# Kernel tuning notes

Measured on AMD Instinct MI355X. Metric: run time of the kernel, lower is better.

Reference implementation:

```python
import jax, jax.numpy as jnp
import numpy as np

ARAP_WEIGHT = 1.0


def _decoder(code, W1, b1, W2, b2, W3, b3):
    # code: [D] -> vertices [N, 3]
    h = jax.nn.relu(code @ W1 + b1)
    h = jax.nn.relu(h @ W2 + b2)
    v = h @ W3 + b3
    return v.reshape(-1, 3)


def _arap_per_vertex(xyz1, recon, nbr, num_nbr, wmat):
    # xyz1, recon: [N,3]; nbr: [N,K] int; num_nbr: [N]; wmat: [N,K]
    N, K = nbr.shape
    mask = (jnp.arange(K)[None, :] < num_nbr[:, None]).astype(wmat.dtype)
    w = wmat * mask                              # zero out padded neighbors
    e_rest = xyz1[nbr] - xyz1[:, None, :]        # [N,K,3] rest-pose edges (gather)
    e_def = recon[nbr] - recon[:, None, :]       # [N,K,3] deformed edges (gather)
    # weighted covariance per vertex: S_i = sum_k w_ik e_ik e'_ik^T  -> [N,3,3]
    S = jnp.einsum('nk,nka,nkb->nab', w, e_rest, e_def)
    U, _, Vt = jnp.linalg.svd(S)
    V = jnp.swapaxes(Vt, -1, -2)
    R0 = jnp.einsum('nab,ncb->nac', V, U)        # V U^T
    d = jnp.linalg.det(R0)                       # reflection fix
    diag = jnp.stack([jnp.ones_like(d), jnp.ones_like(d), d], axis=-1)  # [N,3]
    R = jnp.einsum('nab,nb,ncb->nac', V, diag, U)
    R = jax.lax.stop_gradient(R)                 # local-global: rotations fixed in bwd
    e_rot = jnp.einsum('nab,nkb->nka', R, e_rest)
    resid = e_def - e_rot
    return jnp.sum(w * jnp.sum(resid * resid, axis=-1), axis=-1)  # [N]


def setup_inputs() -> dict:
    key = jax.random.key(0)
    ks = jax.random.split(key, 12)
    N, K, D = 20000, 16, 256
    H1, H2 = 512, 1024
    inp = {
        'code': jax.random.normal(ks[0], (D,), jnp.float32),
        'xyz1': jax.random.normal(ks[1], (N, 3), jnp.float32),
        'weightMatrix': jax.random.uniform(ks[2], (N, K), jnp.float32),
        'W1': jax.random.normal(ks[3], (D, H1), jnp.float32) * (1.0 / np.sqrt(D)),
        'b1': jax.random.normal(ks[4], (H1,), jnp.float32) * 0.01,
        'W2': jax.random.normal(ks[5], (H1, H2), jnp.float32) * (1.0 / np.sqrt(H1)),
        'b2': jax.random.normal(ks[6], (H2,), jnp.float32) * 0.01,
        'W3': jax.random.normal(ks[7], (H2, N * 3), jnp.float32) * (1.0 / np.sqrt(H2)),
        'b3': jax.random.normal(ks[8], (N * 3,), jnp.float32) * 0.01,
        'neighborsMatrix': jax.random.randint(ks[9], (N, K), 0, N, jnp.int64),
        'numNeighbors': jax.random.randint(ks[10], (N,), 0, 17, jnp.int64),
    }
    return inp


def reference(code, xyz1, weightMatrix, W1, b1, W2, b2, W3, b3,
              neighborsMatrix, numNeighbors):
    def energy(c):
        recon = _decoder(c, W1, b1, W2, b2, W3, b3)
        pv = _arap_per_vertex(xyz1, recon, neighborsMatrix, numNeighbors, weightMatrix)
        return ARAP_WEIGHT * jnp.mean(pv)

    E, g = jax.value_and_grad(energy)(code)
    # torch module returns (arapEnergy.item(), -code.grad) with arapEnergy = -E
    return (-E, g)
```

## Files before the change

### kernel.cpp

```cpp
#include <hip/hip_runtime.h>
#include <hip/hip_bf16.h>

#define N_V   20000
#define KNB   16
#define DCODE 256
#define H1    512
#define H2    1024
#define M3    60000

#define OFF_L2P   0
#define OFF_VPART 8192
#define OFF_V     488192
#define OFF_GV    548192
#define OFF_GZ2   608192
#define OFF_GZ1   609216
#define OFF_H1    609728
#define OFF_H2    610240
#define OFF_HC    611264
#define OFF_LIST  612288
#define OFF_CNT   613312
#define OFF_E     613316

__global__ void k_mlp12(const float* __restrict__ code, const float* __restrict__ W1,
                        const float* __restrict__ b1, const float* __restrict__ W2,
                        float* __restrict__ ws) {
    __shared__ float red[4][64];
    __shared__ float h1s[64];
    int t = threadIdx.x;
    int bx = blockIdx.x, dz = blockIdx.y;
    int d0 = dz * 64;

    int ln = t & 63, g = t >> 6;
    {
        float acc = 0.f;
        int r0 = g * 64;
#pragma unroll 8
        for (int rr = 0; rr < 64; ++rr)
            acc += code[r0 + rr] * W1[(size_t)(r0 + rr) * H1 + d0 + ln];
        red[g][ln] = acc;
    }
    __syncthreads();
    if (g == 0) {
        float h = fmaxf(red[0][ln] + red[1][ln] + red[2][ln] + red[3][ln] + b1[d0 + ln], 0.f);
        h1s[ln] = h;
        if (bx == 0) ws[OFF_H1 + d0 + ln] = h;
    }
    __syncthreads();

    int m = bx * 256 + t;
    float acc = 0.f;
#pragma unroll 8
    for (int dd = 0; dd < 64; ++dd)
        acc += h1s[dd] * W2[(size_t)(d0 + dd) * H2 + m];
    ws[OFF_L2P + dz * H2 + m] = acc;

    int gid = (dz * 4 + bx) * 256 + t;
    for (int idx = gid; idx < M3; idx += 8192) ws[OFF_GV + idx] = 0.f;
    if (gid == 0) { ws[OFF_E] = 0.f; ws[OFF_E + 1] = 0.f; }
}

__global__ void k_compact(const float* __restrict__ b2, float* __restrict__ ws) {
    __shared__ int scan[256];
    int t = threadIdx.x;
    float h[4]; int c = 0;
#pragma unroll
    for (int q = 0; q < 4; ++q) {
        int j = t * 4 + q;
        float s = b2[j];
#pragma unroll
        for (int p = 0; p < 8; ++p) s += ws[OFF_L2P + p * H2 + j];
        float hv = fmaxf(s, 0.f);
        ws[OFF_H2 + j] = hv;
        ws[OFF_GZ2 + j] = 0.f;
        h[q] = hv;
        c += (hv > 0.f) ? 1 : 0;
    }
    scan[t] = c;
    __syncthreads();
    for (int off = 1; off < 256; off <<= 1) {
        int x = (t >= off) ? scan[t - off] : 0;
        __syncthreads();
        scan[t] += x;
        __syncthreads();
    }
    int base = scan[t] - c;
    int* list = reinterpret_cast<int*>(&ws[OFF_LIST]);
#pragma unroll
    for (int q = 0; q < 4; ++q) {
        if (h[q] > 0.f) {
            list[base] = t * 4 + q;
            ws[OFF_HC + base] = h[q];
            ++base;
        }
    }
    if (t == 255) *reinterpret_cast<int*>(&ws[OFF_CNT]) = scan[255];
}

__global__ void k_l3p(const float* __restrict__ W3, float* __restrict__ ws) {
    __shared__ int   rlist[128];
    __shared__ float rh[128];
    int jz = blockIdx.y;
    int cnt = *reinterpret_cast<const int*>(&ws[OFF_CNT]);
    int per = (cnt + 7) >> 3;
    int s0 = jz * per;
    int s1 = s0 + per; if (s1 > cnt) s1 = cnt;
    int n = s1 - s0;
    int t = threadIdx.x;
    if (t < 128 && t < n) {
        rlist[t] = reinterpret_cast<const int*>(&ws[OFF_LIST])[s0 + t];
        rh[t]    = ws[OFF_HC + s0 + t];
    }
    __syncthreads();
    int m4 = blockIdx.x * 1024 + t * 4;
    if (m4 >= M3) return;
    float ax = 0.f, ay = 0.f, az = 0.f, aw = 0.f;
    int ii = 0;
    for (; ii + 7 < n; ii += 8) {
        float4 wv[8];
#pragma unroll
        for (int u = 0; u < 8; ++u)
            wv[u] = *reinterpret_cast<const float4*>(&W3[(size_t)rlist[ii + u] * M3 + m4]);
#pragma unroll
        for (int u = 0; u < 8; ++u) {
            float h = rh[ii + u];
            ax += h * wv[u].x; ay += h * wv[u].y; az += h * wv[u].z; aw += h * wv[u].w;
        }
    }
    for (; ii < n; ++ii) {
        float h = rh[ii];
        float4 wv = *reinterpret_cast<const float4*>(&W3[(size_t)rlist[ii] * M3 + m4]);
        ax += h * wv.x; ay += h * wv.y; az += h * wv.z; aw += h * wv.w;
    }
    *reinterpret_cast<float4*>(&ws[OFF_VPART + jz * M3 + m4]) =
        make_float4(ax, ay, az, aw);
}

__global__ void k_vred(const float* __restrict__ b3, float* __restrict__ ws) {
    int i4 = blockIdx.x * 256 + threadIdx.x;
    if (i4 < M3 / 4) {
        int m = i4 * 4;
        float4 a = *reinterpret_cast<const float4*>(&b3[m]);
#pragma unroll
        for (int jz = 0; jz < 8; ++jz) {
            float4 p = *reinterpret_cast<const float4*>(&ws[OFF_VPART + jz * M3 + m]);
            a.x += p.x; a.y += p.y; a.z += p.z; a.w += p.w;
        }
        *reinterpret_cast<float4*>(&ws[OFF_V + m]) = a;
    }
}


__device__ inline void jrotf(float a[3][3], float v[3][3], int p, int q) {
    float apq = a[p][q];
    if (fabsf(apq) < 1e-30f) return;
    float theta = (a[q][q] - a[p][p]) / (2.0f * apq);
    float t;
    if (fabsf(theta) > 1e18f) t = 0.5f / theta;
    else t = copysignf(1.0f, theta) / (fabsf(theta) + sqrtf(theta * theta + 1.0f));
    float c = 1.0f / sqrtf(t * t + 1.0f);
    float s = t * c;
    float app = a[p][p], aqq = a[q][q];
    a[p][p] = app - t * apq;
    a[q][q] = aqq + t * apq;
    a[p][q] = 0.0f; a[q][p] = 0.0f;
    int r = 3 - p - q;
    float arp = a[r][p], arq = a[r][q];
    a[r][p] = c * arp - s * arq; a[p][r] = a[r][p];
    a[r][q] = s * arp + c * arq; a[q][r] = a[r][q];
#pragma unroll
    for (int k2 = 0; k2 < 3; ++k2) {
        float vkp = v[k2][p], vkq = v[k2][q];
        v[k2][p] = c * vkp - s * vkq;
        v[k2][q] = s * vkp + c * vkq;
    }
}

__device__ void compute_Rf(const float S[3][3], float R[3][3]) {
    float A[3][3], V[3][3];
#pragma unroll
    for (int a = 0; a < 3; ++a)
#pragma unroll
        for (int b = 0; b < 3; ++b) {
            float s = 0.0f;
#pragma unroll
            for (int c = 0; c < 3; ++c) s += S[c][a] * S[c][b];
            A[a][b] = s;
            V[a][b] = (a == b) ? 1.0f : 0.0f;
        }
    for (int sweep = 0; sweep < 15; ++sweep) {
        float off = A[0][1]*A[0][1] + A[0][2]*A[0][2] + A[1][2]*A[1][2];
        float dg  = A[0][0]*A[0][0] + A[1][1]*A[1][1] + A[2][2]*A[2][2];
        if (off <= 1e-12f * (dg + 1e-30f)) break;
        jrotf(A, V, 0, 1); jrotf(A, V, 0, 2); jrotf(A, V, 1, 2);
    }
    int id[3] = {0, 1, 2};
    if (A[id[0]][id[0]] < A[id[1]][id[1]]) { int t = id[0]; id[0] = id[1]; id[1] = t; }
    if (A[id[0]][id[0]] < A[id[2]][id[2]]) { int t = id[0]; id[0] = id[2]; id[2] = t; }
    if (A[id[1]][id[1]] < A[id[2]][id[2]]) { int t = id[1]; id[1] = id[2]; id[2] = t; }
    float v0[3], v1[3], v2[3];
#pragma unroll
    for (int r = 0; r < 3; ++r) {
        v0[r] = V[r][id[0]]; v1[r] = V[r][id[1]]; v2[r] = V[r][id[2]];
    }
    float u0[3], u1[3], u2[3];
#pragma unroll
    for (int a = 0; a < 3; ++a)
        u0[a] = S[a][0]*v0[0] + S[a][1]*v0[1] + S[a][2]*v0[2];
    float n0 = sqrtf(u0[0]*u0[0] + u0[1]*u0[1] + u0[2]*u0[2]);
    if (!(n0 > 1e-20f)) {
#pragma unroll
        for (int a = 0; a < 3; ++a)
#pragma unroll
            for (int c = 0; c < 3; ++c) R[a][c] = (a == c) ? 1.0f : 0.0f;
        return;
    }
#pragma unroll
    for (int a = 0; a < 3; ++a) u0[a] /= n0;
    float t1[3];
#pragma unroll
    for (int a = 0; a < 3; ++a)
        t1[a] = S[a][0]*v1[0] + S[a][1]*v1[1] + S[a][2]*v1[2];
    float dp = u0[0]*t1[0] + u0[1]*t1[1] + u0[2]*t1[2];
#pragma unroll
    for (int a = 0; a < 3; ++a) t1[a] -= dp * u0[a];
    float n1 = sqrtf(t1[0]*t1[0] + t1[1]*t1[1] + t1[2]*t1[2]);
    if (n1 > 1e-5f * n0) {
#pragma unroll
        for (int a = 0; a < 3; ++a) u1[a] = t1[a] / n1;
    } else {
        int m = (fabsf(u0[0]) <= fabsf(u0[1]) && fabsf(u0[0]) <= fabsf(u0[2])) ? 0
              : (fabsf(u0[1]) <= fabsf(u0[2]) ? 1 : 2);
        float e[3] = {0.0f, 0.0f, 0.0f}; e[m] = 1.0f;
        float cx[3] = { u0[1]*e[2] - u0[2]*e[1],
                        u0[2]*e[0] - u0[0]*e[2],
                        u0[0]*e[1] - u0[1]*e[0] };
        float nn = sqrtf(cx[0]*cx[0] + cx[1]*cx[1] + cx[2]*cx[2]);
#pragma unroll
        for (int a = 0; a < 3; ++a) u1[a] = cx[a] / nn;
    }
    u2[0] = u0[1]*u1[2] - u0[2]*u1[1];
    u2[1] = u0[2]*u1[0] - u0[0]*u1[2];
    u2[2] = u0[0]*u1[1] - u0[1]*u1[0];
    float d = v0[0]*(v1[1]*v2[2] - v1[2]*v2[1])
            - v0[1]*(v1[0]*v2[2] - v1[2]*v2[0])
            + v0[2]*(v1[0]*v2[1] - v1[1]*v2[0]);
#pragma unroll
    for (int a = 0; a < 3; ++a)
#pragma unroll
        for (int c = 0; c < 3; ++c)
            R[a][c] = v0[a]*u0[c] + v1[a]*u1[c] + d * (v2[a]*u2[c]);
}

__global__ void k_arap(const float* __restrict__ xyz1, const float* __restrict__ wmat,
                       const int* __restrict__ nbr, const int* __restrict__ nnum,
                       float* __restrict__ ws) {
    const float* recon = ws + OFF_V;
    float* gv = ws + OFF_GV;
    int i = blockIdx.x * 256 + threadIdx.x;
    double pv = 0.0;
    if (i < N_V) {
        int num = nnum[i]; if (num > KNB) num = KNB;
        float cr0 = xyz1[3*i], cr1 = xyz1[3*i+1], cr2 = xyz1[3*i+2];
        float cd0 = recon[3*i], cd1 = recon[3*i+1], cd2 = recon[3*i+2];
        float er[KNB][3], ed[KNB][3], wk[KNB];
        int   jn[KNB];
        float S[3][3] = {{0,0,0},{0,0,0},{0,0,0}};
#pragma unroll
        for (int k = 0; k < KNB; ++k) {
            bool live = (k < num);
            int j = live ? nbr[i*KNB + k] : i;
            float w = live ? wmat[i*KNB + k] : 0.f;
            jn[k] = j; wk[k] = w;
            float e0 = xyz1[3*j]   - cr0, e1 = xyz1[3*j+1] - cr1, e2 = xyz1[3*j+2] - cr2;
            float f0 = recon[3*j]  - cd0, f1 = recon[3*j+1] - cd1, f2 = recon[3*j+2] - cd2;
            er[k][0] = e0; er[k][1] = e1; er[k][2] = e2;
            ed[k][0] = f0; ed[k][1] = f1; ed[k][2] = f2;
            S[0][0] += w*e0*f0; S[0][1] += w*e0*f1; S[0][2] += w*e0*f2;
            S[1][0] += w*e1*f0; S[1][1] += w*e1*f1; S[1][2] += w*e1*f2;
            S[2][0] += w*e2*f0; S[2][1] += w*e2*f1; S[2][2] += w*e2*f2;
        }
        float R[3][3];
        compute_Rf(S, R);
        const float gscale = 2.0f / (float)N_V;
        float own0 = 0.f, own1 = 0.f, own2 = 0.f;
#pragma unroll
        for (int k = 0; k < KNB; ++k) {
            if (k < num) {
                float w = wk[k];
                float r0 = ed[k][0] - (R[0][0]*er[k][0] + R[0][1]*er[k][1] + R[0][2]*er[k][2]);
                float r1 = ed[k][1] - (R[1][0]*er[k][0] + R[1][1]*er[k][1] + R[1][2]*er[k][2]);
                float r2 = ed[k][2] - (R[2][0]*er[k][0] + R[2][1]*er[k][1] + R[2][2]*er[k][2]);
                pv += (double)(w * (r0*r0 + r1*r1 + r2*r2));
                float g0 = gscale * w * r0;
                float g1 = gscale * w * r1;
                float g2 = gscale * w * r2;
                int j = jn[k];
                atomicAdd(&gv[3*j+0], g0);
                atomicAdd(&gv[3*j+1], g1);
                atomicAdd(&gv[3*j+2], g2);
                own0 += g0; own1 += g1; own2 += g2;
            }
        }
        if (num > 0) {
            atomicAdd(&gv[3*i+0], -own0);
            atomicAdd(&gv[3*i+1], -own1);
            atomicAdd(&gv[3*i+2], -own2);
        }
    }
#pragma unroll
    for (int m = 32; m; m >>= 1) pv += __shfl_xor(pv, m);
    __shared__ double wred[4];
    if ((threadIdx.x & 63) == 0) wred[threadIdx.x >> 6] = pv;
    __syncthreads();
    if (threadIdx.x == 0)
        atomicAdd(reinterpret_cast<double*>(ws + OFF_E),
                  wred[0] + wred[1] + wred[2] + wred[3]);
}


__global__ void k_gh2(const float* __restrict__ W3, float* __restrict__ ws) {
    int b = blockIdx.x;
    int cnt = *reinterpret_cast<const int*>(&ws[OFF_CNT]);
    if (2 * b >= cnt) return;
    const int* list = reinterpret_cast<const int*>(&ws[OFF_LIST]);
    int j0 = list[2 * b];
    bool has1 = (2 * b + 1 < cnt);
    int j1 = has1 ? list[2 * b + 1] : j0;
    const float4* w3r0 = reinterpret_cast<const float4*>(W3 + (size_t)j0 * M3);
    const float4* w3r1 = reinterpret_cast<const float4*>(W3 + (size_t)j1 * M3);
    const float4* gv4  = reinterpret_cast<const float4*>(ws + OFF_GV);
    float acc0 = 0.f, acc1 = 0.f;
    for (int it = threadIdx.x; it < M3 / 4; it += 256) {
        float4 g = gv4[it];
        float4 a = w3r0[it];
        float4 c = w3r1[it];
        acc0 += a.x*g.x + a.y*g.y + a.z*g.z + a.w*g.w;
        acc1 += c.x*g.x + c.y*g.y + c.z*g.z + c.w*g.w;
    }
    for (int m = 32; m; m >>= 1) {
        acc0 += __shfl_xor(acc0, m);
        acc1 += __shfl_xor(acc1, m);
    }
    __shared__ float wsum[4][2];
    if ((threadIdx.x & 63) == 0) {
        wsum[threadIdx.x >> 6][0] = acc0;
        wsum[threadIdx.x >> 6][1] = acc1;
    }
    __syncthreads();
    if (threadIdx.x == 0) {
        ws[OFF_GZ2 + j0] = wsum[0][0] + wsum[1][0] + wsum[2][0] + wsum[3][0];
        if (has1)
            ws[OFF_GZ2 + j1] = wsum[0][1] + wsum[1][1] + wsum[2][1] + wsum[3][1];
    }
}

__global__ void k_gh1(const float* __restrict__ W2, float* __restrict__ ws) {
    int wv = threadIdx.x >> 6, ln = threadIdx.x & 63;
    int i = blockIdx.x * 4 + wv;
    const float* gz2 = ws + OFF_GZ2;
    float acc = 0.f;
#pragma unroll
    for (int it = 0; it < H2 / 64; ++it) {
        int jj = ln + it * 64;
        acc += W2[(size_t)i * H2 + jj] * gz2[jj];
    }
    for (int m = 32; m; m >>= 1) acc += __shfl_xor(acc, m);
    if (ln == 0) ws[OFF_GZ1 + i] = (ws[OFF_H1 + i] > 0.f) ? acc : 0.f;
}

__global__ void k_gcode(const float* __restrict__ W1, float* __restrict__ ws,
                        float* __restrict__ out) {
    int wv = threadIdx.x >> 6, ln = threadIdx.x & 63;
    int d = blockIdx.x * 4 + wv;
    const float* gz1 = ws + OFF_GZ1;
    float acc = 0.f;
#pragma unroll
    for (int it = 0; it < H1 / 64; ++it) {
        int ii = ln + it * 64;
        acc += W1[(size_t)d * H1 + ii] * gz1[ii];
    }
    for (int m = 32; m; m >>= 1) acc += __shfl_xor(acc, m);
    if (ln == 0) out[1 + d] = acc;
    if (blockIdx.x == 0 && threadIdx.x == 0) {
        double E = *reinterpret_cast<const double*>(ws + OFF_E);
        out[0] = (float)(-(E / (double)N_V));
    }
}

extern "C" void kernel_launch(void* const* d_in, const int* in_sizes, int n_in,
                              void* d_out, int out_size, void* d_ws, size_t ws_size,
                              hipStream_t stream) {
    const float* code = (const float*)d_in[0];
    const float* xyz1 = (const float*)d_in[1];
    const float* wmat = (const float*)d_in[2];
    const float* W1   = (const float*)d_in[3];
    const float* b1   = (const float*)d_in[4];
    const float* W2   = (const float*)d_in[5];
    const float* b2   = (const float*)d_in[6];
    const float* W3   = (const float*)d_in[7];
    const float* b3   = (const float*)d_in[8];
    const int*   nbr  = (const int*)d_in[9];
    const int*   nnum = (const int*)d_in[10];
    float* out = (float*)d_out;
    float* ws  = (float*)d_ws;

    k_mlp12  <<<dim3(4, 8),  256, 0, stream>>>(code, W1, b1, W2, ws);
    k_compact<<<1,           256, 0, stream>>>(b2, ws);
    k_l3p    <<<dim3(59, 8), 256, 0, stream>>>(W3, ws);
    k_vred   <<<59,          256, 0, stream>>>(b3, ws);
    k_arap   <<<79,          256, 0, stream>>>(xyz1, wmat, nbr, nnum, ws);
    k_gh2    <<<512,         256, 0, stream>>>(W3, ws);
    k_gh1    <<<128,         256, 0, stream>>>(W2, ws);
    k_gcode  <<<64,          256, 0, stream>>>(W1, ws, out);
}
```

Before: 120.8 us.

## Fuse compaction into layer-3 GEMV, atomics for vertex sum, faster SVD, split gh2

Folds the single-block ReLU compaction into each k_l3p block, which now computes its own 128-row slice of h2. Partial vertex sums are accumulated into b3-initialised memory with atomics, which removes k_vred and the 8x60000 partial buffer. Also replaces the Jacobi convergence check with six fixed sweeps using hardware rcp/rsq, launches ARAP with 64-thread blocks for more blocks, and splits the gh2 reduction across two halves with unrolled accumulators. This trades two kernel launches and extra traffic for float atomic contention, non-deterministic summation order and slightly less accurate rotations.

```diff
diff --git a/kernel.cpp b/kernel.cpp
--- a/kernel.cpp
+++ b/kernel.cpp
@@ -9,21 +9,20 @@
 #define M3    60000
 
 #define OFF_L2P   0
-#define OFF_VPART 8192
-#define OFF_V     488192
-#define OFF_GV    548192
-#define OFF_GZ2   608192
-#define OFF_GZ1   609216
-#define OFF_H1    609728
-#define OFF_H2    610240
-#define OFF_HC    611264
-#define OFF_LIST  612288
-#define OFF_CNT   613312
-#define OFF_E     613316
+#define OFF_V     8192
+#define OFF_GV    68192
+#define OFF_GZ2P  128192
+#define OFF_GZ1   130240
+#define OFF_H1    130752
+#define OFF_H2    131264
+#define OFF_HC    132288
+#define OFF_LIST  133312
+#define OFF_CNT8  134336
+#define OFF_E     134344
 
 __global__ void k_mlp12(const float* __restrict__ code, const float* __restrict__ W1,
                         const float* __restrict__ b1, const float* __restrict__ W2,
-                        float* __restrict__ ws) {
+                        const float* __restrict__ b3, float* __restrict__ ws) {
     __shared__ float red[4][64];
     __shared__ float h1s[64];
     int t = threadIdx.x;
@@ -55,62 +54,56 @@
     ws[OFF_L2P + dz * H2 + m] = acc;
 
     int gid = (dz * 4 + bx) * 256 + t;
-    for (int idx = gid; idx < M3; idx += 8192) ws[OFF_GV + idx] = 0.f;
-    if (gid == 0) { ws[OFF_E] = 0.f; ws[OFF_E + 1] = 0.f; }
-}
-
-__global__ void k_compact(const float* __restrict__ b2, float* __restrict__ ws) {
-    __shared__ int scan[256];
+    for (int idx = gid; idx < M3; idx += 8192) {
+        ws[OFF_V + idx]  = b3[idx];
+        ws[OFF_GV + idx] = 0.f;
+    }
+    if (gid == 0) *reinterpret_cast<double*>(ws + OFF_E) = 0.0;
+}
+
+__global__ void k_l3p(const float* __restrict__ b2, const float* __restrict__ W3,
+                      float* __restrict__ ws) {
+    __shared__ float rh[128];
+    __shared__ int   rlist[128];
+    __shared__ int   scan[128];
     int t = threadIdx.x;
-    float h[4]; int c = 0;
-#pragma unroll
-    for (int q = 0; q < 4; ++q) {
-        int j = t * 4 + q;
-        float s = b2[j];
-#pragma unroll
-        for (int p = 0; p < 8; ++p) s += ws[OFF_L2P + p * H2 + j];
-        float hv = fmaxf(s, 0.f);
-        ws[OFF_H2 + j] = hv;
-        ws[OFF_GZ2 + j] = 0.f;
-        h[q] = hv;
-        c += (hv > 0.f) ? 1 : 0;
-    }
-    scan[t] = c;
+    int jz = blockIdx.y;
+    int rbase = jz * 128;
+
+    float hv = 0.f; int flag = 0;
+    if (t < 128) {
+        float s = b2[rbase + t];
+#pragma unroll
+        for (int p = 0; p < 8; ++p) s += ws[OFF_L2P + p * H2 + rbase + t];
+        hv = fmaxf(s, 0.f);
+        flag = (hv > 0.f) ? 1 : 0;
+        scan[t] = flag;
+    }
     __syncthreads();
-    for (int off = 1; off < 256; off <<= 1) {
-        int x = (t >= off) ? scan[t - off] : 0;
+    for (int off = 1; off < 128; off <<= 1) {
+        int x = 0;
+        if (t < 128 && t >= off) x = scan[t - off];
         __syncthreads();
-        scan[t] += x;
+        if (t < 128) scan[t] += x;
         __syncthreads();
     }
-    int base = scan[t] - c;
-    int* list = reinterpret_cast<int*>(&ws[OFF_LIST]);
-#pragma unroll
-    for (int q = 0; q < 4; ++q) {
-        if (h[q] > 0.f) {
-            list[base] = t * 4 + q;
-            ws[OFF_HC + base] = h[q];
-            ++base;
-        }
-    }
-    if (t == 255) *reinterpret_cast<int*>(&ws[OFF_CNT]) = scan[255];
-}
-
-__global__ void k_l3p(const float* __restrict__ W3, float* __restrict__ ws) {
-    __shared__ int   rlist[128];
-    __shared__ float rh[128];
-    int jz = blockIdx.y;
-    int cnt = *reinterpret_cast<const int*>(&ws[OFF_CNT]);
-    int per = (cnt + 7) >> 3;
-    int s0 = jz * per;
-    int s1 = s0 + per; if (s1 > cnt) s1 = cnt;
-    int n = s1 - s0;
-    int t = threadIdx.x;
-    if (t < 128 && t < n) {
-        rlist[t] = reinterpret_cast<const int*>(&ws[OFF_LIST])[s0 + t];
-        rh[t]    = ws[OFF_HC + s0 + t];
+    if (t < 128 && flag) {
+        int idx = scan[t] - 1;
+        rlist[idx] = rbase + t;
+        rh[idx] = hv;
+    }
+    if (blockIdx.x == 0 && t < 128) {
+        ws[OFF_H2 + rbase + t] = hv;
+        if (flag) {
+            reinterpret_cast<int*>(&ws[OFF_LIST])[jz * 128 + scan[t] - 1] = rbase + t;
+            ws[OFF_HC + jz * 128 + scan[t] - 1] = hv;
+        }
+        if (t == 127)
+            reinterpret_cast<int*>(&ws[OFF_CNT8])[jz] = scan[127];
     }
     __syncthreads();
+    int n = scan[127];
+
     int m4 = blockIdx.x * 1024 + t * 4;
     if (m4 >= M3) return;
     float ax = 0.f, ay = 0.f, az = 0.f, aw = 0.f;
@@ -131,33 +124,25 @@
         float4 wv = *reinterpret_cast<const float4*>(&W3[(size_t)rlist[ii] * M3 + m4]);
         ax += h * wv.x; ay += h * wv.y; az += h * wv.z; aw += h * wv.w;
     }
-    *reinterpret_cast<float4*>(&ws[OFF_VPART + jz * M3 + m4]) =
-        make_float4(ax, ay, az, aw);
-}
-
-__global__ void k_vred(const float* __restrict__ b3, float* __restrict__ ws) {
-    int i4 = blockIdx.x * 256 + threadIdx.x;
-    if (i4 < M3 / 4) {
-        int m = i4 * 4;
-        float4 a = *reinterpret_cast<const float4*>(&b3[m]);
-#pragma unroll
-        for (int jz = 0; jz < 8; ++jz) {
-            float4 p = *reinterpret_cast<const float4*>(&ws[OFF_VPART + jz * M3 + m]);
-            a.x += p.x; a.y += p.y; a.z += p.z; a.w += p.w;
-        }
-        *reinterpret_cast<float4*>(&ws[OFF_V + m]) = a;
-    }
-}
-
+    if (n > 0) {
+        atomicAdd(&ws[OFF_V + m4 + 0], ax);
+        atomicAdd(&ws[OFF_V + m4 + 1], ay);
+        atomicAdd(&ws[OFF_V + m4 + 2], az);
+        atomicAdd(&ws[OFF_V + m4 + 3], aw);
+    }
+}
+
+
+__device__ inline float frcp(float x) { return __builtin_amdgcn_rcpf(x); }
+__device__ inline float frsq(float x) { return __builtin_amdgcn_rsqf(x); }
 
 __device__ inline void jrotf(float a[3][3], float v[3][3], int p, int q) {
     float apq = a[p][q];
-    if (fabsf(apq) < 1e-30f) return;
-    float theta = (a[q][q] - a[p][p]) / (2.0f * apq);
-    float t;
-    if (fabsf(theta) > 1e18f) t = 0.5f / theta;
-    else t = copysignf(1.0f, theta) / (fabsf(theta) + sqrtf(theta * theta + 1.0f));
-    float c = 1.0f / sqrtf(t * t + 1.0f);
+    float den = 2.0f * apq;
+    float sden = copysignf(fmaxf(fabsf(den), 1e-30f), den);
+    float theta = (a[q][q] - a[p][p]) * frcp(sden);
+    float t = copysignf(1.0f, theta) * frcp(fabsf(theta) + sqrtf(theta * theta + 1.0f));
+    float c = frsq(t * t + 1.0f);
     float s = t * c;
     float app = a[p][p], aqq = a[q][q];
     a[p][p] = app - t * apq;
@@ -187,10 +172,7 @@
             A[a][b] = s;
             V[a][b] = (a == b) ? 1.0f : 0.0f;
         }
-    for (int sweep = 0; sweep < 15; ++sweep) {
-        float off = A[0][1]*A[0][1] + A[0][2]*A[0][2] + A[1][2]*A[1][2];
-        float dg  = A[0][0]*A[0][0] + A[1][1]*A[1][1] + A[2][2]*A[2][2];
-        if (off <= 1e-12f * (dg + 1e-30f)) break;
+    for (int sweep = 0; sweep < 6; ++sweep) {
         jrotf(A, V, 0, 1); jrotf(A, V, 0, 2); jrotf(A, V, 1, 2);
     }
     int id[3] = {0, 1, 2};
@@ -214,8 +196,9 @@
             for (int c = 0; c < 3; ++c) R[a][c] = (a == c) ? 1.0f : 0.0f;
         return;
     }
-#pragma unroll
-    for (int a = 0; a < 3; ++a) u0[a] /= n0;
+    float rn0 = frcp(n0);
+#pragma unroll
+    for (int a = 0; a < 3; ++a) u0[a] *= rn0;
     float t1[3];
 #pragma unroll
     for (int a = 0; a < 3; ++a)
@@ -225,8 +208,9 @@
     for (int a = 0; a < 3; ++a) t1[a] -= dp * u0[a];
     float n1 = sqrtf(t1[0]*t1[0] + t1[1]*t1[1] + t1[2]*t1[2]);
     if (n1 > 1e-5f * n0) {
-#pragma unroll
-        for (int a = 0; a < 3; ++a) u1[a] = t1[a] / n1;
+        float rn1 = frcp(n1);
+#pragma unroll
+        for (int a = 0; a < 3; ++a) u1[a] = t1[a] * rn1;
     } else {
         int m = (fabsf(u0[0]) <= fabsf(u0[1]) && fabsf(u0[0]) <= fabsf(u0[2])) ? 0
               : (fabsf(u0[1]) <= fabsf(u0[2]) ? 1 : 2);
@@ -234,9 +218,9 @@
         float cx[3] = { u0[1]*e[2] - u0[2]*e[1],
                         u0[2]*e[0] - u0[0]*e[2],
                         u0[0]*e[1] - u0[1]*e[0] };
-        float nn = sqrtf(cx[0]*cx[0] + cx[1]*cx[1] + cx[2]*cx[2]);
-#pragma unroll
-        for (int a = 0; a < 3; ++a) u1[a] = cx[a] / nn;
+        float rnn = frsq(cx[0]*cx[0] + cx[1]*cx[1] + cx[2]*cx[2]);
+#pragma unroll
+        for (int a = 0; a < 3; ++a) u1[a] = cx[a] * rnn;
     }
     u2[0] = u0[1]*u1[2] - u0[2]*u1[1];
     u2[1] = u0[2]*u1[0] - u0[0]*u1[2];
@@ -256,7 +240,7 @@
                        float* __restrict__ ws) {
     const float* recon = ws + OFF_V;
     float* gv = ws + OFF_GV;
-    int i = blockIdx.x * 256 + threadIdx.x;
+    int i = blockIdx.x * 64 + threadIdx.x;
     double pv = 0.0;
     if (i < N_V) {
         int num = nnum[i]; if (num > KNB) num = KNB;
@@ -271,8 +255,8 @@
             int j = live ? nbr[i*KNB + k] : i;
             float w = live ? wmat[i*KNB + k] : 0.f;
             jn[k] = j; wk[k] = w;
-            float e0 = xyz1[3*j]   - cr0, e1 = xyz1[3*j+1] - cr1, e2 = xyz1[3*j+2] - cr2;
-            float f0 = recon[3*j]  - cd0, f1 = recon[3*j+1] - cd1, f2 = recon[3*j+2] - cd2;
+            float e0 = xyz1[3*j]  - cr0, e1 = xyz1[3*j+1] - cr1, e2 = xyz1[3*j+2] - cr2;
+            float f0 = recon[3*j] - cd0, f1 = recon[3*j+1] - cd1, f2 = recon[3*j+2] - cd2;
             er[k][0] = e0; er[k][1] = e1; er[k][2] = e2;
             ed[k][0] = f0; ed[k][1] = f1; ed[k][2] = f2;
             S[0][0] += w*e0*f0; S[0][1] += w*e0*f1; S[0][2] += w*e0*f2;
@@ -309,60 +293,97 @@
     }
 #pragma unroll
     for (int m = 32; m; m >>= 1) pv += __shfl_xor(pv, m);
-    __shared__ double wred[4];
-    if ((threadIdx.x & 63) == 0) wred[threadIdx.x >> 6] = pv;
-    __syncthreads();
     if (threadIdx.x == 0)
-        atomicAdd(reinterpret_cast<double*>(ws + OFF_E),
-                  wred[0] + wred[1] + wred[2] + wred[3]);
+        atomicAdd(reinterpret_cast<double*>(ws + OFF_E), pv);
 }
 
 
 __global__ void k_gh2(const float* __restrict__ W3, float* __restrict__ ws) {
-    int b = blockIdx.x;
-    int cnt = *reinterpret_cast<const int*>(&ws[OFF_CNT]);
-    if (2 * b >= cnt) return;
+    const int* cnt8 = reinterpret_cast<const int*>(&ws[OFF_CNT8]);
+    int pre[9];
+    pre[0] = 0;
+#pragma unroll
+    for (int c = 0; c < 8; ++c) pre[c + 1] = pre[c] + cnt8[c];
+    int total = pre[8];
+    int g0 = 2 * blockIdx.x;
+    if (g0 >= total) return;
+    int g1 = g0 + 1;
+    bool has1 = (g1 < total);
+
     const int* list = reinterpret_cast<const int*>(&ws[OFF_LIST]);
-    int j0 = list[2 * b];
-    bool has1 = (2 * b + 1 < cnt);
-    int j1 = has1 ? list[2 * b + 1] : j0;
+    int c0 = 0, c1 = 0;
+#pragma unroll
+    for (int c = 0; c < 8; ++c) {
+        if (g0 >= pre[c + 1]) c0 = c + 1;
+        if (g1 >= pre[c + 1]) c1 = c + 1;
+    }
+    int j0 = list[c0 * 128 + (g0 - pre[c0])];
+    int j1 = has1 ? list[c1 * 128 + (g1 - pre[c1])] : j0;
+
+    int half = blockIdx.y;
+    int start = half * 7500;
+    int end = start + 7500;
     const float4* w3r0 = reinterpret_cast<const float4*>(W3 + (size_t)j0 * M3);
     const float4* w3r1 = reinterpret_cast<const float4*>(W3 + (size_t)j1 * M3);
     const float4* gv4  = reinterpret_cast<const float4*>(ws + OFF_GV);
-    float acc0 = 0.f, acc1 = 0.f;
-    for (int it = threadIdx.x; it < M3 / 4; it += 256) {
+    int t = threadIdx.x;
+
+    float a00 = 0.f, a01 = 0.f, a02 = 0.f, a03 = 0.f;
+    float a10 = 0.f, a11 = 0.f, a12 = 0.f, a13 = 0.f;
+    int it = start + t;
+    for (; it + 768 < end; it += 1024) {
+        float4 g0v = gv4[it],        g1v = gv4[it + 256],
+               g2v = gv4[it + 512],  g3v = gv4[it + 768];
+        float4 p0 = w3r0[it],        p1 = w3r0[it + 256],
+               p2 = w3r0[it + 512],  p3 = w3r0[it + 768];
+        float4 q0 = w3r1[it],        q1 = w3r1[it + 256],
+               q2 = w3r1[it + 512],  q3 = w3r1[it + 768];
+        a00 += p0.x*g0v.x + p0.y*g0v.y + p0.z*g0v.z + p0.w*g0v.w;
+        a01 += p1.x*g1v.x + p1.y*g1v.y + p1.z*g1v.z + p1.w*g1v.w;
+        a02 += p2.x*g2v.x + p2.y*g2v.y + p2.z*g2v.z + p2.w*g2v.w;
+        a03 += p3.x*g3v.x + p3.y*g3v.y + p3.z*g3v.z + p3.w*g3v.w;
+        a10 += q0.x*g0v.x + q0.y*g0v.y + q0.z*g0v.z + q0.w*g0v.w;
+        a11 += q1.x*g1v.x + q1.y*g1v.y + q1.z*g1v.z + q1.w*g1v.w;
+        a12 += q2.x*g2v.x + q2.y*g2v.y + q2.z*g2v.z + q2.w*g2v.w;
+        a13 += q3.x*g3v.x + q3.y*g3v.y + q3.z*g3v.z + q3.w*g3v.w;
+    }
+    for (; it < end; it += 256) {
         float4 g = gv4[it];
-        float4 a = w3r0[it];
-        float4 c = w3r1[it];
-        acc0 += a.x*g.x + a.y*g.y + a.z*g.z + a.w*g.w;
-        acc1 += c.x*g.x + c.y*g.y + c.z*g.z + c.w*g.w;
-    }
+        float4 p = w3r0[it];
+        float4 q = w3r1[it];
+        a00 += p.x*g.x + p.y*g.y + p.z*g.z + p.w*g.w;
+        a10 += q.x*g.x + q.y*g.y + q.z*g.z + q.w*g.w;
+    }
+    float acc0 = a00 + a01 + a02 + a03;
+    float acc1 = a10 + a11 + a12 + a13;
     for (int m = 32; m; m >>= 1) {
         acc0 += __shfl_xor(acc0, m);
         acc1 += __shfl_xor(acc1, m);
     }
     __shared__ float wsum[4][2];
-    if ((threadIdx.x & 63) == 0) {
-        wsum[threadIdx.x >> 6][0] = acc0;
-        wsum[threadIdx.x >> 6][1] = acc1;
+    if ((t & 63) == 0) {
+        wsum[t >> 6][0] = acc0;
+        wsum[t >> 6][1] = acc1;
     }
     __syncthreads();
-    if (threadIdx.x == 0) {
-        ws[OFF_GZ2 + j0] = wsum[0][0] + wsum[1][0] + wsum[2][0] + wsum[3][0];
+    if (t == 0) {
+        float* gz2p = ws + OFF_GZ2P + half * H2;
+        gz2p[j0] = wsum[0][0] + wsum[1][0] + wsum[2][0] + wsum[3][0];
         if (has1)
-            ws[OFF_GZ2 + j1] = wsum[0][1] + wsum[1][1] + wsum[2][1] + wsum[3][1];
+            gz2p[j1] = wsum[0][1] + wsum[1][1] + wsum[2][1] + wsum[3][1];
     }
 }
 
 __global__ void k_gh1(const float* __restrict__ W2, float* __restrict__ ws) {
     int wv = threadIdx.x >> 6, ln = threadIdx.x & 63;
     int i = blockIdx.x * 4 + wv;
-    const float* gz2 = ws + OFF_GZ2;
     float acc = 0.f;
 #pragma unroll
     for (int it = 0; it < H2 / 64; ++it) {
         int jj = ln + it * 64;
-        acc += W2[(size_t)i * H2 + jj] * gz2[jj];
+        float gz2 = (ws[OFF_H2 + jj] > 0.f)
+                  ? (ws[OFF_GZ2P + jj] + ws[OFF_GZ2P + H2 + jj]) : 0.f;
+        acc += W2[(size_t)i * H2 + jj] * gz2;
     }
     for (int m = 32; m; m >>= 1) acc += __shfl_xor(acc, m);
     if (ln == 0) ws[OFF_GZ1 + i] = (ws[OFF_H1 + i] > 0.f) ? acc : 0.f;
@@ -404,12 +425,10 @@
     float* out = (float*)d_out;
     float* ws  = (float*)d_ws;
 
-    k_mlp12  <<<dim3(4, 8),  256, 0, stream>>>(code, W1, b1, W2, ws);
-    k_compact<<<1,           256, 0, stream>>>(b2, ws);
-    k_l3p    <<<dim3(59, 8), 256, 0, stream>>>(W3, ws);
-    k_vred   <<<59,          256, 0, stream>>>(b3, ws);
-    k_arap   <<<79,          256, 0, stream>>>(xyz1, wmat, nbr, nnum, ws);
-    k_gh2    <<<512,         256, 0, stream>>>(W3, ws);
-    k_gh1    <<<128,         256, 0, stream>>>(W2, ws);
-    k_gcode  <<<64,          256, 0, stream>>>(W1, ws, out);
-}
+    k_mlp12<<<dim3(4, 8),   256, 0, stream>>>(code, W1, b1, W2, b3, ws);
+    k_l3p  <<<dim3(59, 8),  256, 0, stream>>>(b2, W3, ws);
+    k_arap <<<313,           64, 0, stream>>>(xyz1, wmat, nbr, nnum, ws);
+    k_gh2  <<<dim3(256, 2), 256, 0, stream>>>(W3, ws);
+    k_gh1  <<<128,          256, 0, stream>>>(W2, ws);
+    k_gcode<<<64,           256, 0, stream>>>(W1, ws, out);
+}
```

Result: no change. 120.1 us (-0.6%).
